# Optimization experiments

Measured on AMD Instinct MI355X. Metric: run time of the kernel, lower is better.

Reference implementation:

```python
import jax, jax.numpy as jnp
import numpy as np

N_NODES = 10000
IN_F = 512
OUT_F = 512
N_EDGES = 160000
GRID_SIZE = 5      # KAN spline grid intervals
SPLINE_ORDER = 3   # cubic B-splines -> GRID_SIZE + SPLINE_ORDER = 8 basis fns per input dim
ALPHA = 0.2        # LeakyReLU negative slope


def _grid():
    # uniform extended grid on [-1, 1], shape [GRID_SIZE + 2*SPLINE_ORDER + 1]
    step = 2.0 / GRID_SIZE
    return jnp.arange(-SPLINE_ORDER, GRID_SIZE + SPLINE_ORDER + 1, dtype=jnp.float32) * step - 1.0


def _b_splines(x, grid):
    # x: [N, in] -> basis: [N, in, GRID_SIZE + SPLINE_ORDER] via Cox-de Boor recursion
    x = x[..., None]  # [N, in, 1]
    bases = ((x >= grid[:-1]) & (x < grid[1:])).astype(x.dtype)  # order-0
    for p in range(1, SPLINE_ORDER + 1):
        left = (x - grid[: -(p + 1)]) / (grid[p:-1] - grid[: -(p + 1)]) * bases[..., :-1]
        right = (grid[p + 1:] - x) / (grid[p + 1:] - grid[1:-p]) * bases[..., 1:]
        bases = left + right
    return bases


def setup_inputs() -> dict:
    key = jax.random.key(0)
    k1, k2, k3, k4, k5, k6 = jax.random.split(key, 6)
    h = jax.random.normal(k1, (N_NODES, IN_F), dtype=jnp.float32)
    edge_index = jax.random.randint(k2, (2, N_EDGES), 0, N_NODES, dtype=jnp.int64)
    xav = float(np.sqrt(2.0 / (IN_F + OUT_F))) * 1.414
    W = jax.random.normal(k3, (IN_F, OUT_F), dtype=jnp.float32) * xav
    a = jax.random.normal(k4, (2 * OUT_F, 1), dtype=jnp.float32) * float(np.sqrt(2.0 / (2 * OUT_F + 1)))
    base_w = jax.random.normal(k5, (OUT_F, IN_F), dtype=jnp.float32) * xav
    n_coef = GRID_SIZE + SPLINE_ORDER
    spline_w = jax.random.normal(k6, (OUT_F, IN_F, n_coef), dtype=jnp.float32) * 0.1
    return {"h": h, "W": W, "a": a, "base_w": base_w, "spline_w": spline_w, "edge_index": edge_index}


def reference(h, W, a, base_w, spline_w, edge_index):
    HW = h @ W  # [N, out]
    row, col = edge_index[0], edge_index[1]
    # a_input @ a == HW_i @ a[:out] + HW_j @ a[out:] (same math, avoids the concat)
    s = HW @ a[:OUT_F, 0]   # [N]
    t = HW @ a[OUT_F:, 0]   # [N]
    e = jax.nn.leaky_relu(s[row] + t[col], negative_slope=ALPHA)  # [E]
    # segment softmax keyed on destination (row)
    m = jax.ops.segment_max(e, row, num_segments=N_NODES)
    ex = jnp.exp(e - m[row])
    den = jax.ops.segment_sum(ex, row, num_segments=N_NODES)
    att = ex / den[row]
    # dropout p=0.6 is identity in eval mode
    # scatter-add aggregation of raw features h[col] (as in the source)
    agg = jax.ops.segment_sum(att[:, None] * h[col], row, num_segments=N_NODES)  # [N, in]
    # KANLayer: silu base path + B-spline path (efficient-KAN formulation)
    grid = _grid()
    basis = _b_splines(agg, grid)  # [N, in, n_coef]
    out = jax.nn.silu(agg) @ base_w.T + jnp.einsum('nip,oip->no', basis, spline_w)
    return out
```

## Files before the change

### kernel.cpp

```cpp
#include <hip/hip_runtime.h>
#include <hip/hip_bf16.h>
#include <math.h>

#define N_NODES 10000
#define IN_F 512
#define OUT_F 512
#define N_EDGES 160000
#define K_SPLINE 4096
#define K_TOTAL 4608
#define NBK 144
#define NBM 628
#define ALPHA 0.2f

typedef __attribute__((ext_vector_type(8))) short short8;
typedef __attribute__((ext_vector_type(4))) float f32x4;
typedef unsigned short ushort_t;
typedef unsigned long long u64;

__device__ __forceinline__ unsigned bfpair(float a, float b) {
    __hip_bfloat162 h2 = __float22bfloat162_rn(make_float2(a, b));
    return *reinterpret_cast<unsigned*>(&h2);
}
__device__ __forceinline__ float bflo(unsigned u) { return __uint_as_float(u << 16); }
__device__ __forceinline__ float bfhi(unsigned u) { return __uint_as_float(u & 0xffff0000u); }

__device__ __forceinline__ float silu_f(float x) {
    return x / (1.f + __expf(-x));
}

__device__ __forceinline__ uint4 spline_window(float x) {
    float xc = (x + 2.2f) * 2.5f;
    float fc = floorf(xc);
    int c = (int)fc;
    float u = xc - fc;
    float omu = 1.f - u;
    float u2 = u * u, u3 = u2 * u;
    float n0 = (1.f / 6.f) * omu * omu * omu;
    float n1 = 0.5f * u3 - u2 + (2.f / 3.f);
    float n2 = -0.5f * u3 + 0.5f * u2 + 0.5f * u + (1.f / 6.f);
    float n3 = (1.f / 6.f) * u3;
    u64 V = (u64)bfpair(n0, n1) | ((u64)bfpair(n2, n3) << 32);
    int sh = (c - 3) * 16;
    u64 lo, hi;
    if (c < 0 || c > 10)    { lo = 0; hi = 0; }
    else if (sh >= 64)      { lo = 0; hi = V << (sh - 64); }
    else if (sh > 0)        { lo = V << sh; hi = V >> (64 - sh); }
    else if (sh == 0)       { lo = V; hi = 0; }
    else                    { lo = V >> (-sh); hi = 0; }
    uint4 pk;
    pk.x = (unsigned)lo; pk.y = (unsigned)(lo >> 32);
    pk.z = (unsigned)hi; pk.w = (unsigned)(hi >> 32);
    return pk;
}

__global__ void fused1_kernel(const float* __restrict__ W, const float* __restrict__ a,
                              float* __restrict__ wa0, float* __restrict__ wa1,
                              const float* __restrict__ base_w, const float* __restrict__ spline_w,
                              ushort_t* __restrict__ Bt,
                              const float* __restrict__ h, ushort_t* __restrict__ hb,
                              const int* __restrict__ ei, int* __restrict__ deg) {
    int b = blockIdx.x;
    int tid = threadIdx.x;
    if (b < 128) {
        int w = tid >> 6, l = tid & 63;
        int i = b * 4 + w;
        float s0 = 0.f, s1 = 0.f;
        #pragma unroll
        for (int oo = 0; oo < 8; ++oo) {
            int o = l + oo * 64;
            float wv = W[(size_t)i * OUT_F + o];
            s0 += wv * a[o];
            s1 += wv * a[OUT_F + o];
        }
        #pragma unroll
        for (int off = 32; off > 0; off >>= 1) {
            s0 += __shfl_down(s0, off, 64);
            s1 += __shfl_down(s1, off, 64);
        }
        if (l == 0) { wa0[i] = s0; wa1[i] = s1; }
    } else if (b < 1280) {
        int gid = (b - 128) * 256 + tid;
        int o = gid / 576;
        int kb8 = gid - o * 576;
        int k0 = kb8 * 8;
        float4 x0, x1;
        if (k0 < K_SPLINE) {
            const float4* p = (const float4*)(spline_w + (size_t)o * K_SPLINE + k0);
            x0 = p[0]; x1 = p[1];
        } else {
            const float4* p = (const float4*)(base_w + (size_t)o * IN_F + (k0 - K_SPLINE));
            x0 = p[0]; x1 = p[1];
        }
        int frag = (k0 >> 5) * 32 + (o >> 4);
        int lane = ((kb8 & 3) << 4) + (o & 15);
        uint4 pk;
        pk.x = bfpair(x0.x, x0.y);
        pk.y = bfpair(x0.z, x0.w);
        pk.z = bfpair(x1.x, x1.y);
        pk.w = bfpair(x1.z, x1.w);
        *(uint4*)(Bt + ((size_t)frag * 64 + lane) * 8) = pk;
    } else if (b < 3780) {
        int id = (b - 1280) * 256 + tid;
        const float4* p = (const float4*)(h + (size_t)id * 8);
        float4 a0 = p[0], a1 = p[1];
        uint4 pk;
        pk.x = bfpair(a0.x, a0.y);
        pk.y = bfpair(a0.z, a0.w);
        pk.z = bfpair(a1.x, a1.y);
        pk.w = bfpair(a1.z, a1.w);
        *(uint4*)(hb + (size_t)id * 8) = pk;
    } else {
        int k = (b - 3780) * 256 + tid;
        if (k < N_EDGES) atomicAdd(&deg[ei[k]], 1);
    }
}

__global__ void fused2_kernel(const float* __restrict__ h, const float* __restrict__ wa0,
                              const float* __restrict__ wa1,
                              float* __restrict__ s, float* __restrict__ t,
                              const int* __restrict__ deg, int* __restrict__ off,
                              int* __restrict__ cursor) {
    __shared__ int sb[256];
    int b = blockIdx.x;
    int tid = threadIdx.x;
    if (b < 2500) {
        int w = tid >> 6, l = tid & 63;
        int n = b * 4 + w;
        const float4* hp = (const float4*)(h + (size_t)n * IN_F);
        float4 hA = hp[l], hB = hp[l + 64];
        float4 wA0 = ((const float4*)wa0)[l], wB0 = ((const float4*)wa0)[l + 64];
        float4 wA1 = ((const float4*)wa1)[l], wB1 = ((const float4*)wa1)[l + 64];
        float ss = hA.x*wA0.x + hA.y*wA0.y + hA.z*wA0.z + hA.w*wA0.w
                 + hB.x*wB0.x + hB.y*wB0.y + hB.z*wB0.z + hB.w*wB0.w;
        float tt = hA.x*wA1.x + hA.y*wA1.y + hA.z*wA1.z + hA.w*wA1.w
                 + hB.x*wB1.x + hB.y*wB1.y + hB.z*wB1.z + hB.w*wB1.w;
        #pragma unroll
        for (int o = 32; o > 0; o >>= 1) {
            ss += __shfl_down(ss, o, 64);
            tt += __shfl_down(tt, o, 64);
        }
        if (l == 0) { s[n] = ss; t[n] = tt; }
    } else {
        int d[40];
        int tot = 0;
        #pragma unroll
        for (int j = 0; j < 40; ++j) {
            int idx = tid * 40 + j;
            d[j] = (idx < N_NODES) ? deg[idx] : 0;
            tot += d[j];
        }
        sb[tid] = tot;
        __syncthreads();
        for (int sd = 1; sd < 256; sd <<= 1) {
            int v = (tid >= sd) ? sb[tid - sd] : 0;
            __syncthreads();
            sb[tid] += v;
            __syncthreads();
        }
        int run = (tid > 0) ? sb[tid - 1] : 0;
        #pragma unroll
        for (int j = 0; j < 40; ++j) {
            int idx = tid * 40 + j;
            if (idx < N_NODES) { off[idx] = run; cursor[idx] = run; }
            run += d[j];
        }
        if (tid == 255) off[N_NODES] = sb[255];
    }
}

__global__ void fill_kernel(const int* __restrict__ ei, int* __restrict__ cursor,
                            int* __restrict__ csr_col) {
    int k = blockIdx.x * 256 + threadIdx.x;
    if (k < N_EDGES) {
        int r = ei[k];
        int c = ei[N_EDGES + k];
        int p = atomicAdd(&cursor[r], 1);
        csr_col[p] = c;
    }
}

__global__ __launch_bounds__(256) void agg_kernel(
    const ushort_t* __restrict__ hb, const float* __restrict__ s,
    const float* __restrict__ t, const int* __restrict__ off,
    const int* __restrict__ csr, float* __restrict__ agg) {
    int w = threadIdx.x >> 6, l = threadIdx.x & 63;
    int n = blockIdx.x * 4 + w;
    int e0 = off[n], e1 = off[n + 1];
    float sn = s[n];

    float m = -1e30f, den = 0.f;
    for (int k = e0 + l; k < e1; k += 64) {
        float v = sn + t[csr[k]];
        v = (v >= 0.f) ? v : ALPHA * v;
        float mn = fmaxf(m, v);
        den = den * __expf(m - mn) + __expf(v - mn);
        m = mn;
    }
    #pragma unroll
    for (int o = 1; o < 64; o <<= 1) {
        float m2 = __shfl_xor(m, o, 64);
        float d2 = __shfl_xor(den, o, 64);
        float mn = fmaxf(m, m2);
        den = den * __expf(m - mn) + d2 * __expf(m2 - mn);
        m = mn;
    }
    float inv = (den > 0.f) ? 1.f / den : 0.f;

    float acc[8] = {0.f, 0.f, 0.f, 0.f, 0.f, 0.f, 0.f, 0.f};
    const ushort_t* hbl = hb + l * 8;
    for (int base = e0; base < e1; base += 64) {
        int cnt = e1 - base; if (cnt > 64) cnt = 64;
        int c = 0; float att = 0.f;
        if (l < cnt) {
            c = csr[base + l];
            float v = sn + t[c];
            v = (v >= 0.f) ? v : ALPHA * v;
            att = __expf(v - m) * inv;
        }
        #pragma unroll 4
        for (int j = 0; j < cnt; ++j) {
            float aj = __shfl(att, j, 64);
            int cj = __shfl(c, j, 64);
            uint4 u = *(const uint4*)(hbl + (size_t)cj * IN_F);
            acc[0] = fmaf(aj, bflo(u.x), acc[0]);
            acc[1] = fmaf(aj, bfhi(u.x), acc[1]);
            acc[2] = fmaf(aj, bflo(u.y), acc[2]);
            acc[3] = fmaf(aj, bfhi(u.y), acc[3]);
            acc[4] = fmaf(aj, bflo(u.z), acc[4]);
            acc[5] = fmaf(aj, bfhi(u.z), acc[5]);
            acc[6] = fmaf(aj, bflo(u.w), acc[6]);
            acc[7] = fmaf(aj, bfhi(u.w), acc[7]);
        }
    }
    float* arow = agg + (size_t)n * IN_F + l * 8;
    *(float4*)arow       = make_float4(acc[0], acc[1], acc[2], acc[3]);
    *(float4*)(arow + 4) = make_float4(acc[4], acc[5], acc[6], acc[7]);
}

__global__ void expand_kernel(const float* __restrict__ agg, ushort_t* __restrict__ Xf) {
    int id = blockIdx.x * 256 + threadIdx.x;
    int l = id & 63;
    int fid = id >> 6;
    int nb = fid / NBK;
    int kb = fid - nb * NBK;
    int n = nb * 16 + (l & 15);
    uint4 pk = make_uint4(0u, 0u, 0u, 0u);
    if (n < N_NODES) {
        if (kb < 128) {
            int dim = kb * 4 + (l >> 4);
            pk = spline_window(agg[(size_t)n * IN_F + dim]);
        } else {
            const float* ap = agg + (size_t)n * IN_F + (kb - 128) * 32 + (l >> 4) * 8;
            float4 x0 = *(const float4*)ap;
            float4 x1 = *(const float4*)(ap + 4);
            pk.x = bfpair(silu_f(x0.x), silu_f(x0.y));
            pk.y = bfpair(silu_f(x0.z), silu_f(x0.w));
            pk.z = bfpair(silu_f(x1.x), silu_f(x1.y));
            pk.w = bfpair(silu_f(x1.z), silu_f(x1.w));
        }
    }
    *(uint4*)(Xf + (size_t)id * 8) = pk;
}

__global__ __launch_bounds__(256, 3) void kan_gemm2(
    const ushort_t* __restrict__ Xf, const ushort_t* __restrict__ Bt,
    float* __restrict__ out) {
    __shared__ ushort_t A_lds[2][4][4][64][8];

    int d = blockIdx.x;
    int g = d >> 5, r = d & 31;
    int bm = g * 8 + (r & 7), bn = r >> 3;
    if (bm >= 157) return;
    int tid = threadIdx.x, w = tid >> 6, l = tid & 63;
    int wc16 = bn * 8 + w * 2;

    f32x4 acc[4][2];
    #pragma unroll
    for (int m = 0; m < 4; ++m)
        #pragma unroll
        for (int nf = 0; nf < 2; ++nf)
            acc[m][nf] = (f32x4){0.f, 0.f, 0.f, 0.f};

    short8 b0[8], b1[8];

    auto stage = [&](int j, int pb) {
        #pragma unroll
        for (int ks = 0; ks < 4; ++ks) {
            const ushort_t* src = Xf + (((size_t)(bm * 4 + w) * NBK + 4 * j + ks) * 64 + l) * 8;
            __builtin_amdgcn_global_load_lds(
                (const __attribute__((address_space(1))) unsigned int*)src,
                (__attribute__((address_space(3))) unsigned int*)&A_lds[pb][ks][w][0][0],
                16, 0, 0);
        }
    };
    auto loadB = [&](int j, short8 (&b)[8]) {
        #pragma unroll
        for (int ks = 0; ks < 4; ++ks) {
            int kb = 4 * j + ks;
            b[ks * 2 + 0] = *(const short8*)(Bt + ((size_t)(kb * 32 + wc16)     * 64 + l) * 8);
            b[ks * 2 + 1] = *(const short8*)(Bt + ((size_t)(kb * 32 + wc16 + 1) * 64 + l) * 8);
        }
    };
    auto compute = [&](int pb, short8 (&b)[8]) {
        #pragma unroll
        for (int ks = 0; ks < 4; ++ks)
            #pragma unroll
            for (int m = 0; m < 4; ++m) {
                short8 af = *(const short8*)&A_lds[pb][ks][m][l][0];
                acc[m][0] = __builtin_amdgcn_mfma_f32_16x16x32_bf16(af, b[ks * 2 + 0], acc[m][0], 0, 0, 0);
                acc[m][1] = __builtin_amdgcn_mfma_f32_16x16x32_bf16(af, b[ks * 2 + 1], acc[m][1], 0, 0, 0);
            }
    };

    stage(0, 0);
    loadB(0, b0);
    __syncthreads();
    for (int j = 0; j < 36; j += 2) {
        if (j + 1 < 36) { stage(j + 1, 1); loadB(j + 1, b1); }
        compute(0, b0);
        __syncthreads();
        if (j + 2 < 36) { stage(j + 2, 0); loadB(j + 2, b0); }
        compute(1, b1);
        __syncthreads();
    }

    #pragma unroll
    for (int m = 0; m < 4; ++m) {
        int r0 = bm * 64 + m * 16 + ((l >> 4) << 2);
        #pragma unroll
        for (int nf = 0; nf < 2; ++nf) {
            int colg = bn * 128 + w * 32 + nf * 16 + (l & 15);
            #pragma unroll
            for (int jr = 0; jr < 4; ++jr) {
                int rr = r0 + jr;
                if (rr < N_NODES) out[(size_t)rr * OUT_F + colg] = acc[m][nf][jr];
            }
        }
    }
}

extern "C" void kernel_launch(void* const* d_in, const int* in_sizes, int n_in,
                              void* d_out, int out_size, void* d_ws, size_t ws_size,
                              hipStream_t stream) {
    const float* h        = (const float*)d_in[0];
    const float* W        = (const float*)d_in[1];
    const float* a        = (const float*)d_in[2];
    const float* base_w   = (const float*)d_in[3];
    const float* spline_w = (const float*)d_in[4];
    const int*   ei       = (const int*)d_in[5];
    float* out = (float*)d_out;

    char* ws = (char*)d_ws;
    size_t cur = 0;
    auto alloc = [&](size_t bytes) -> void* {
        void* p = ws + cur;
        cur += (bytes + 255) & ~(size_t)255;
        return p;
    };
    float* wa0    = (float*)alloc(512 * 4);
    float* wa1    = (float*)alloc(512 * 4);
    float* s      = (float*)alloc(N_NODES * 4);
    float* t      = (float*)alloc(N_NODES * 4);
    int*   deg    = (int*)alloc(N_NODES * 4);
    int*   offp   = (int*)alloc((N_NODES + 1) * 4);
    int*   cursor = (int*)alloc(N_NODES * 4);
    int*   csr    = (int*)alloc(N_EDGES * 4);
    float* agg    = (float*)alloc((size_t)N_NODES * IN_F * 4);
    ushort_t* Bt  = (ushort_t*)alloc((size_t)K_TOTAL * OUT_F * 2);
    ushort_t* hb  = (ushort_t*)alloc((size_t)N_NODES * IN_F * 2);
    ushort_t* Xf  = (ushort_t*)alloc((size_t)NBM * NBK * 64 * 16);
    if (cur > ws_size) return;

    hipMemsetAsync(deg, 0, N_NODES * 4, stream);
    fused1_kernel<<<4405, 256, 0, stream>>>(W, a, wa0, wa1, base_w, spline_w, Bt, h, hb, ei, deg);
    fused2_kernel<<<2501, 256, 0, stream>>>(h, wa0, wa1, s, t, deg, offp, cursor);
    fill_kernel<<<(N_EDGES + 255) / 256, 256, 0, stream>>>(ei, cursor, csr);
    agg_kernel<<<2500, 256, 0, stream>>>(hb, s, t, offp, csr, agg);
    expand_kernel<<<NBM * NBK * 64 / 256, 256, 0, stream>>>(agg, Xf);
    kan_gemm2<<<640, 256, 0, stream>>>(Xf, Bt, out);
}
```

Before: 168.3 us.

## Fuse aggregation with spline/silu expansion via LDS and retile KAN GEMM

Aggregation and feature expansion now run in one kernel. Each block aggregates 16 nodes into shared memory and then writes the bf16 spline-window and silu operand tiles straight into Xf. This removes the fp32 agg buffer's global write and read-back, plus one kernel launch. The KAN GEMM is also retiled from 64x128 to 128x64 output tiles, with each wave computing 2x4 MFMA fragments, and NBM is padded so the grid divides evenly. The padded Xf rows are never written, but their outputs are masked on store.

```diff
diff --git a/kernel.cpp b/kernel.cpp
--- a/kernel.cpp
+++ b/kernel.cpp
@@ -9,7 +9,7 @@
 #define K_SPLINE 4096
 #define K_TOTAL 4608
 #define NBK 144
-#define NBM 628
+#define NBM 632
 #define ALPHA 0.2f
 
 typedef __attribute__((ext_vector_type(8))) short short8;
@@ -179,78 +179,78 @@
     }
 }
 
-__global__ __launch_bounds__(256) void agg_kernel(
+__global__ __launch_bounds__(256) void aggexp_kernel(
     const ushort_t* __restrict__ hb, const float* __restrict__ s,
     const float* __restrict__ t, const int* __restrict__ off,
-    const int* __restrict__ csr, float* __restrict__ agg) {
+    const int* __restrict__ csr, ushort_t* __restrict__ Xf) {
+    __shared__ float AL[16][516];
     int w = threadIdx.x >> 6, l = threadIdx.x & 63;
-    int n = blockIdx.x * 4 + w;
-    int e0 = off[n], e1 = off[n + 1];
-    float sn = s[n];
-
-    float m = -1e30f, den = 0.f;
-    for (int k = e0 + l; k < e1; k += 64) {
-        float v = sn + t[csr[k]];
-        v = (v >= 0.f) ? v : ALPHA * v;
-        float mn = fmaxf(m, v);
-        den = den * __expf(m - mn) + __expf(v - mn);
-        m = mn;
-    }
-    #pragma unroll
-    for (int o = 1; o < 64; o <<= 1) {
-        float m2 = __shfl_xor(m, o, 64);
-        float d2 = __shfl_xor(den, o, 64);
-        float mn = fmaxf(m, m2);
-        den = den * __expf(m - mn) + d2 * __expf(m2 - mn);
-        m = mn;
-    }
-    float inv = (den > 0.f) ? 1.f / den : 0.f;
-
-    float acc[8] = {0.f, 0.f, 0.f, 0.f, 0.f, 0.f, 0.f, 0.f};
-    const ushort_t* hbl = hb + l * 8;
-    for (int base = e0; base < e1; base += 64) {
-        int cnt = e1 - base; if (cnt > 64) cnt = 64;
-        int c = 0; float att = 0.f;
-        if (l < cnt) {
-            c = csr[base + l];
-            float v = sn + t[c];
+    int nb = blockIdx.x;
+
+    for (int q = 0; q < 4; ++q) {
+        int n = nb * 16 + w * 4 + q;
+        int e0 = off[n], e1 = off[n + 1];
+        float sn = s[n];
+
+        float m = -1e30f, den = 0.f;
+        for (int k = e0 + l; k < e1; k += 64) {
+            float v = sn + t[csr[k]];
             v = (v >= 0.f) ? v : ALPHA * v;
-            att = __expf(v - m) * inv;
-        }
-        #pragma unroll 4
-        for (int j = 0; j < cnt; ++j) {
-            float aj = __shfl(att, j, 64);
-            int cj = __shfl(c, j, 64);
-            uint4 u = *(const uint4*)(hbl + (size_t)cj * IN_F);
-            acc[0] = fmaf(aj, bflo(u.x), acc[0]);
-            acc[1] = fmaf(aj, bfhi(u.x), acc[1]);
-            acc[2] = fmaf(aj, bflo(u.y), acc[2]);
-            acc[3] = fmaf(aj, bfhi(u.y), acc[3]);
-            acc[4] = fmaf(aj, bflo(u.z), acc[4]);
-            acc[5] = fmaf(aj, bfhi(u.z), acc[5]);
-            acc[6] = fmaf(aj, bflo(u.w), acc[6]);
-            acc[7] = fmaf(aj, bfhi(u.w), acc[7]);
-        }
-    }
-    float* arow = agg + (size_t)n * IN_F + l * 8;
-    *(float4*)arow       = make_float4(acc[0], acc[1], acc[2], acc[3]);
-    *(float4*)(arow + 4) = make_float4(acc[4], acc[5], acc[6], acc[7]);
-}
-
-__global__ void expand_kernel(const float* __restrict__ agg, ushort_t* __restrict__ Xf) {
-    int id = blockIdx.x * 256 + threadIdx.x;
-    int l = id & 63;
-    int fid = id >> 6;
-    int nb = fid / NBK;
-    int kb = fid - nb * NBK;
-    int n = nb * 16 + (l & 15);
-    uint4 pk = make_uint4(0u, 0u, 0u, 0u);
-    if (n < N_NODES) {
+            float mn = fmaxf(m, v);
+            den = den * __expf(m - mn) + __expf(v - mn);
+            m = mn;
+        }
+        #pragma unroll
+        for (int o = 1; o < 64; o <<= 1) {
+            float m2 = __shfl_xor(m, o, 64);
+            float d2 = __shfl_xor(den, o, 64);
+            float mn = fmaxf(m, m2);
+            den = den * __expf(m - mn) + d2 * __expf(m2 - mn);
+            m = mn;
+        }
+        float inv = (den > 0.f) ? 1.f / den : 0.f;
+
+        float acc[8] = {0.f, 0.f, 0.f, 0.f, 0.f, 0.f, 0.f, 0.f};
+        const ushort_t* hbl = hb + l * 8;
+        for (int base = e0; base < e1; base += 64) {
+            int cnt = e1 - base; if (cnt > 64) cnt = 64;
+            int c = 0; float att = 0.f;
+            if (l < cnt) {
+                c = csr[base + l];
+                float v = sn + t[c];
+                v = (v >= 0.f) ? v : ALPHA * v;
+                att = __expf(v - m) * inv;
+            }
+            #pragma unroll 4
+            for (int j = 0; j < cnt; ++j) {
+                float aj = __shfl(att, j, 64);
+                int cj = __shfl(c, j, 64);
+                uint4 u = *(const uint4*)(hbl + (size_t)cj * IN_F);
+                acc[0] = fmaf(aj, bflo(u.x), acc[0]);
+                acc[1] = fmaf(aj, bfhi(u.x), acc[1]);
+                acc[2] = fmaf(aj, bflo(u.y), acc[2]);
+                acc[3] = fmaf(aj, bfhi(u.y), acc[3]);
+                acc[4] = fmaf(aj, bflo(u.z), acc[4]);
+                acc[5] = fmaf(aj, bfhi(u.z), acc[5]);
+                acc[6] = fmaf(aj, bflo(u.w), acc[6]);
+                acc[7] = fmaf(aj, bfhi(u.w), acc[7]);
+            }
+        }
+        float* row = &AL[w * 4 + q][l * 8];
+        #pragma unroll
+        for (int j = 0; j < 8; ++j) row[j] = acc[j];
+    }
+    __syncthreads();
+
+    #pragma unroll 1
+    for (int i = 0; i < 36; ++i) {
+        int kb = w + 4 * i;
+        uint4 pk;
         if (kb < 128) {
             int dim = kb * 4 + (l >> 4);
-            pk = spline_window(agg[(size_t)n * IN_F + dim]);
+            pk = spline_window(AL[l & 15][dim]);
         } else {
-            const float* ap = agg + (size_t)n * IN_F + (kb - 128) * 32 + (l >> 4) * 8;
+            const float* ap = &AL[l & 15][(kb - 128) * 32 + (l >> 4) * 8];
             float4 x0 = *(const float4*)ap;
             float4 x1 = *(const float4*)(ap + 4);
             pk.x = bfpair(silu_f(x0.x), silu_f(x0.y));
@@ -258,82 +258,83 @@
             pk.z = bfpair(silu_f(x1.x), silu_f(x1.y));
             pk.w = bfpair(silu_f(x1.z), silu_f(x1.w));
         }
-    }
-    *(uint4*)(Xf + (size_t)id * 8) = pk;
-}
-
-__global__ __launch_bounds__(256, 3) void kan_gemm2(
+        *(uint4*)(Xf + ((size_t)(nb * NBK + kb) * 64 + l) * 8) = pk;
+    }
+}
+
+__global__ __launch_bounds__(256, 3) void kan_gemm3(
     const ushort_t* __restrict__ Xf, const ushort_t* __restrict__ Bt,
     float* __restrict__ out) {
-    __shared__ ushort_t A_lds[2][4][4][64][8];
+    __shared__ ushort_t A_lds[2][2][8][64][8];
 
     int d = blockIdx.x;
-    int g = d >> 5, r = d & 31;
-    int bm = g * 8 + (r & 7), bn = r >> 3;
-    if (bm >= 157) return;
+    int bm = d >> 3, bn = d & 7;
     int tid = threadIdx.x, w = tid >> 6, l = tid & 63;
-    int wc16 = bn * 8 + w * 2;
-
-    f32x4 acc[4][2];
+
+    f32x4 acc[2][4];
     #pragma unroll
-    for (int m = 0; m < 4; ++m)
-        #pragma unroll
-        for (int nf = 0; nf < 2; ++nf)
-            acc[m][nf] = (f32x4){0.f, 0.f, 0.f, 0.f};
+    for (int mm = 0; mm < 2; ++mm)
+        #pragma unroll
+        for (int nf = 0; nf < 4; ++nf)
+            acc[mm][nf] = (f32x4){0.f, 0.f, 0.f, 0.f};
 
     short8 b0[8], b1[8];
 
     auto stage = [&](int j, int pb) {
         #pragma unroll
-        for (int ks = 0; ks < 4; ++ks) {
-            const ushort_t* src = Xf + (((size_t)(bm * 4 + w) * NBK + 4 * j + ks) * 64 + l) * 8;
+        for (int i = 0; i < 4; ++i) {
+            int fi = i * 4 + w;
+            int kb_l = fi >> 3, nb_l = fi & 7;
+            const ushort_t* src = Xf + (((size_t)(bm * 8 + nb_l) * NBK + 2 * j + kb_l) * 64 + l) * 8;
             __builtin_amdgcn_global_load_lds(
                 (const __attribute__((address_space(1))) unsigned int*)src,
-                (__attribute__((address_space(3))) unsigned int*)&A_lds[pb][ks][w][0][0],
+                (__attribute__((address_space(3))) unsigned int*)&A_lds[pb][kb_l][nb_l][0][0],
                 16, 0, 0);
         }
     };
     auto loadB = [&](int j, short8 (&b)[8]) {
         #pragma unroll
-        for (int ks = 0; ks < 4; ++ks) {
-            int kb = 4 * j + ks;
-            b[ks * 2 + 0] = *(const short8*)(Bt + ((size_t)(kb * 32 + wc16)     * 64 + l) * 8);
-            b[ks * 2 + 1] = *(const short8*)(Bt + ((size_t)(kb * 32 + wc16 + 1) * 64 + l) * 8);
-        }
+        for (int ks = 0; ks < 2; ++ks)
+            #pragma unroll
+            for (int nf = 0; nf < 4; ++nf) {
+                int kb = 2 * j + ks;
+                b[ks * 4 + nf] = *(const short8*)(Bt + ((size_t)(kb * 32 + bn * 4 + nf) * 64 + l) * 8);
+            }
     };
     auto compute = [&](int pb, short8 (&b)[8]) {
         #pragma unroll
-        for (int ks = 0; ks < 4; ++ks)
+        for (int ks = 0; ks < 2; ++ks)
             #pragma unroll
-            for (int m = 0; m < 4; ++m) {
-                short8 af = *(const short8*)&A_lds[pb][ks][m][l][0];
-                acc[m][0] = __builtin_amdgcn_mfma_f32_16x16x32_bf16(af, b[ks * 2 + 0], acc[m][0], 0, 0, 0);
-                acc[m][1] = __builtin_amdgcn_mfma_f32_16x16x32_bf16(af, b[ks * 2 + 1], acc[m][1], 0, 0, 0);
+            for (int mm = 0; mm < 2; ++mm) {
+                short8 af = *(const short8*)&A_lds[pb][ks][w * 2 + mm][l][0];
+                #pragma unroll
+                for (int nf = 0; nf < 4; ++nf)
+                    acc[mm][nf] = __builtin_amdgcn_mfma_f32_16x16x32_bf16(af, b[ks * 4 + nf], acc[mm][nf], 0, 0, 0);
             }
     };
 
     stage(0, 0);
     loadB(0, b0);
     __syncthreads();
-    for (int j = 0; j < 36; j += 2) {
-        if (j + 1 < 36) { stage(j + 1, 1); loadB(j + 1, b1); }
+    for (int j = 0; j < 72; j += 2) {
+        stage(j + 1, 1); loadB(j + 1, b1);
         compute(0, b0);
         __syncthreads();
-        if (j + 2 < 36) { stage(j + 2, 0); loadB(j + 2, b0); }
+        if (j + 2 < 72) { stage(j + 2, 0); loadB(j + 2, b0); }
         compute(1, b1);
         __syncthreads();
     }
 
     #pragma unroll
-    for (int m = 0; m < 4; ++m) {
-        int r0 = bm * 64 + m * 16 + ((l >> 4) << 2);
-        #pragma unroll
-        for (int nf = 0; nf < 2; ++nf) {
-            int colg = bn * 128 + w * 32 + nf * 16 + (l & 15);
+    for (int mm = 0; mm < 2; ++mm) {
+        int r0 = bm * 128 + w * 32 + mm * 16 + ((l >> 4) << 2);
+        #pragma unroll
+        for (int nf = 0; nf < 4; ++nf) {
+            int colg = bn * 64 + nf * 16 + (l & 15);
             #pragma unroll
             for (int jr = 0; jr < 4; ++jr) {
                 int rr = r0 + jr;
-                if (rr < N_NODES) out[(size_t)rr * OUT_F + colg] = acc[m][nf][jr];
+                if (rr < N_NODES) out[(size_t)rr * OUT_F + colg] = acc[mm][nf][jr];
             }
         }
     }
@@ -365,7 +366,6 @@
     int*   offp   = (int*)alloc((N_NODES + 1) * 4);
     int*   cursor = (int*)alloc(N_NODES * 4);
     int*   csr    = (int*)alloc(N_EDGES * 4);
-    float* agg    = (float*)alloc((size_t)N_NODES * IN_F * 4);
     ushort_t* Bt  = (ushort_t*)alloc((size_t)K_TOTAL * OUT_F * 2);
     ushort_t* hb  = (ushort_t*)alloc((size_t)N_NODES * IN_F * 2);
     ushort_t* Xf  = (ushort_t*)alloc((size_t)NBM * NBK * 64 * 16);
@@ -375,7 +375,6 @@
     fused1_kernel<<<4405, 256, 0, stream>>>(W, a, wa0, wa1, base_w, spline_w, Bt, h, hb, ei, deg);
     fused2_kernel<<<2501, 256, 0, stream>>>(h, wa0, wa1, s, t, deg, offp, cursor);
     fill_kernel<<<(N_EDGES + 255) / 256, 256, 0, stream>>>(ei, cursor, csr);
-    agg_kernel<<<2500, 256, 0, stream>>>(hb, s, t, offp, csr, agg);
-    expand_kernel<<<NBM * NBK * 64 / 256, 256, 0, stream>>>(agg, Xf);
-    kan_gemm2<<<640, 256, 0, stream>>>(Xf, Bt, out);
-}
+    aggexp_kernel<<<625, 256, 0, stream>>>(hb, s, t, offp, csr, Xf);
+    kan_gemm3<<<632, 256, 0, stream>>>(Xf, Bt, out);
+}
```

Result: slower. 239.9 us (+42.6%).

## Fuse attention aggregation with spline expansion through LDS and remap GEMM tiles

Applied to the files above, without the earlier changes.

The aggregation and expansion kernels become one kernel. Each block aggregates 16 nodes into a shared-memory tile, then builds the spline and SiLU bf16 operand rows straight from LDS. This removes the fp32 agg buffer, with its full global write and read-back, and one kernel launch. The cost is fewer blocks, each wave handling 4 nodes in sequence, which may hide gather latency less well. The GEMM block-to-tile mapping is also changed to a 2x4 grouping with 632 blocks, which alters L2 reuse.

```diff
diff --git a/kernel.cpp b/kernel.cpp
--- a/kernel.cpp
+++ b/kernel.cpp
@@ -179,78 +179,78 @@
     }
 }
 
-__global__ __launch_bounds__(256) void agg_kernel(
+__global__ __launch_bounds__(256) void aggexp_kernel(
     const ushort_t* __restrict__ hb, const float* __restrict__ s,
     const float* __restrict__ t, const int* __restrict__ off,
-    const int* __restrict__ csr, float* __restrict__ agg) {
+    const int* __restrict__ csr, ushort_t* __restrict__ Xf) {
+    __shared__ float AL[16][516];
     int w = threadIdx.x >> 6, l = threadIdx.x & 63;
-    int n = blockIdx.x * 4 + w;
-    int e0 = off[n], e1 = off[n + 1];
-    float sn = s[n];
-
-    float m = -1e30f, den = 0.f;
-    for (int k = e0 + l; k < e1; k += 64) {
-        float v = sn + t[csr[k]];
-        v = (v >= 0.f) ? v : ALPHA * v;
-        float mn = fmaxf(m, v);
-        den = den * __expf(m - mn) + __expf(v - mn);
-        m = mn;
-    }
-    #pragma unroll
-    for (int o = 1; o < 64; o <<= 1) {
-        float m2 = __shfl_xor(m, o, 64);
-        float d2 = __shfl_xor(den, o, 64);
-        float mn = fmaxf(m, m2);
-        den = den * __expf(m - mn) + d2 * __expf(m2 - mn);
-        m = mn;
-    }
-    float inv = (den > 0.f) ? 1.f / den : 0.f;
-
-    float acc[8] = {0.f, 0.f, 0.f, 0.f, 0.f, 0.f, 0.f, 0.f};
-    const ushort_t* hbl = hb + l * 8;
-    for (int base = e0; base < e1; base += 64) {
-        int cnt = e1 - base; if (cnt > 64) cnt = 64;
-        int c = 0; float att = 0.f;
-        if (l < cnt) {
-            c = csr[base + l];
-            float v = sn + t[c];
+    int nb = blockIdx.x;
+
+    for (int q = 0; q < 4; ++q) {
+        int n = nb * 16 + w * 4 + q;
+        int e0 = off[n], e1 = off[n + 1];
+        float sn = s[n];
+
+        float m = -1e30f, den = 0.f;
+        for (int k = e0 + l; k < e1; k += 64) {
+            float v = sn + t[csr[k]];
             v = (v >= 0.f) ? v : ALPHA * v;
-            att = __expf(v - m) * inv;
-        }
-        #pragma unroll 4
-        for (int j = 0; j < cnt; ++j) {
-            float aj = __shfl(att, j, 64);
-            int cj = __shfl(c, j, 64);
-            uint4 u = *(const uint4*)(hbl + (size_t)cj * IN_F);
-            acc[0] = fmaf(aj, bflo(u.x), acc[0]);
-            acc[1] = fmaf(aj, bfhi(u.x), acc[1]);
-            acc[2] = fmaf(aj, bflo(u.y), acc[2]);
-            acc[3] = fmaf(aj, bfhi(u.y), acc[3]);
-            acc[4] = fmaf(aj, bflo(u.z), acc[4]);
-            acc[5] = fmaf(aj, bfhi(u.z), acc[5]);
-            acc[6] = fmaf(aj, bflo(u.w), acc[6]);
-            acc[7] = fmaf(aj, bfhi(u.w), acc[7]);
-        }
-    }
-    float* arow = agg + (size_t)n * IN_F + l * 8;
-    *(float4*)arow       = make_float4(acc[0], acc[1], acc[2], acc[3]);
-    *(float4*)(arow + 4) = make_float4(acc[4], acc[5], acc[6], acc[7]);
-}
-
-__global__ void expand_kernel(const float* __restrict__ agg, ushort_t* __restrict__ Xf) {
-    int id = blockIdx.x * 256 + threadIdx.x;
-    int l = id & 63;
-    int fid = id >> 6;
-    int nb = fid / NBK;
-    int kb = fid - nb * NBK;
-    int n = nb * 16 + (l & 15);
-    uint4 pk = make_uint4(0u, 0u, 0u, 0u);
-    if (n < N_NODES) {
+            float mn = fmaxf(m, v);
+            den = den * __expf(m - mn) + __expf(v - mn);
+            m = mn;
+        }
+        #pragma unroll
+        for (int o = 1; o < 64; o <<= 1) {
+            float m2 = __shfl_xor(m, o, 64);
+            float d2 = __shfl_xor(den, o, 64);
+            float mn = fmaxf(m, m2);
+            den = den * __expf(m - mn) + d2 * __expf(m2 - mn);
+            m = mn;
+        }
+        float inv = (den > 0.f) ? 1.f / den : 0.f;
+
+        float acc[8] = {0.f, 0.f, 0.f, 0.f, 0.f, 0.f, 0.f, 0.f};
+        const ushort_t* hbl = hb + l * 8;
+        for (int base = e0; base < e1; base += 64) {
+            int cnt = e1 - base; if (cnt > 64) cnt = 64;
+            int c = 0; float att = 0.f;
+            if (l < cnt) {
+                c = csr[base + l];
+                float v = sn + t[c];
+                v = (v >= 0.f) ? v : ALPHA * v;
+                att = __expf(v - m) * inv;
+            }
+            #pragma unroll 4
+            for (int j = 0; j < cnt; ++j) {
+                float aj = __shfl(att, j, 64);
+                int cj = __shfl(c, j, 64);
+                uint4 u = *(const uint4*)(hbl + (size_t)cj * IN_F);
+                acc[0] = fmaf(aj, bflo(u.x), acc[0]);
+                acc[1] = fmaf(aj, bfhi(u.x), acc[1]);
+                acc[2] = fmaf(aj, bflo(u.y), acc[2]);
+                acc[3] = fmaf(aj, bfhi(u.y), acc[3]);
+                acc[4] = fmaf(aj, bflo(u.z), acc[4]);
+                acc[5] = fmaf(aj, bfhi(u.z), acc[5]);
+                acc[6] = fmaf(aj, bflo(u.w), acc[6]);
+                acc[7] = fmaf(aj, bfhi(u.w), acc[7]);
+            }
+        }
+        float* row = &AL[w * 4 + q][l * 8];
+        #pragma unroll
+        for (int j = 0; j < 8; ++j) row[j] = acc[j];
+    }
+    __syncthreads();
+
+    #pragma unroll 1
+    for (int i = 0; i < 36; ++i) {
+        int kb = w + 4 * i;
+        uint4 pk;
         if (kb < 128) {
             int dim = kb * 4 + (l >> 4);
-            pk = spline_window(agg[(size_t)n * IN_F + dim]);
+            pk = spline_window(AL[l & 15][dim]);
         } else {
-            const float* ap = agg + (size_t)n * IN_F + (kb - 128) * 32 + (l >> 4) * 8;
+            const float* ap = &AL[l & 15][(kb - 128) * 32 + (l >> 4) * 8];
             float4 x0 = *(const float4*)ap;
             float4 x1 = *(const float4*)(ap + 4);
             pk.x = bfpair(silu_f(x0.x), silu_f(x0.y));
@@ -258,8 +258,8 @@
             pk.z = bfpair(silu_f(x1.x), silu_f(x1.y));
             pk.w = bfpair(silu_f(x1.z), silu_f(x1.w));
         }
-    }
-    *(uint4*)(Xf + (size_t)id * 8) = pk;
+        *(uint4*)(Xf + ((size_t)(nb * NBK + kb) * 64 + l) * 8) = pk;
+    }
 }
 
 __global__ __launch_bounds__(256, 3) void kan_gemm2(
@@ -268,8 +268,8 @@
     __shared__ ushort_t A_lds[2][4][4][64][8];
 
     int d = blockIdx.x;
-    int g = d >> 5, r = d & 31;
-    int bm = g * 8 + (r & 7), bn = r >> 3;
+    int q = d >> 3, x = d & 7;
+    int bm = q * 2 + (x >> 2), bn = x & 3;
     if (bm >= 157) return;
     int tid = threadIdx.x, w = tid >> 6, l = tid & 63;
     int wc16 = bn * 8 + w * 2;
@@ -365,7 +365,6 @@
     int*   offp   = (int*)alloc((N_NODES + 1) * 4);
     int*   cursor = (int*)alloc(N_NODES * 4);
     int*   csr    = (int*)alloc(N_EDGES * 4);
-    float* agg    = (float*)alloc((size_t)N_NODES * IN_F * 4);
     ushort_t* Bt  = (ushort_t*)alloc((size_t)K_TOTAL * OUT_F * 2);
     ushort_t* hb  = (ushort_t*)alloc((size_t)N_NODES * IN_F * 2);
     ushort_t* Xf  = (ushort_t*)alloc((size_t)NBM * NBK * 64 * 16);
@@ -375,7 +374,6 @@
     fused1_kernel<<<4405, 256, 0, stream>>>(W, a, wa0, wa1, base_w, spline_w, Bt, h, hb, ei, deg);
     fused2_kernel<<<2501, 256, 0, stream>>>(h, wa0, wa1, s, t, deg, offp, cursor);
     fill_kernel<<<(N_EDGES + 255) / 256, 256, 0, stream>>>(ei, cursor, csr);
-    agg_kernel<<<2500, 256, 0, stream>>>(hb, s, t, offp, csr, agg);
-    expand_kernel<<<NBM * NBK * 64 / 256, 256, 0, stream>>>(agg, Xf);
-    kan_gemm2<<<640, 256, 0, stream>>>(Xf, Bt, out);
-}
+    aggexp_kernel<<<625, 256, 0, stream>>>(hb, s, t, offp, csr, Xf);
+    kan_gemm2<<<632, 256, 0, stream>>>(Xf, Bt, out);
+}
```

After: 188.4 us. 12.0% more time.
